# Performance work log

Measured on AMD Instinct MI355X. Metric: run time of the kernel, lower is better.

## Reference

```python
import jax, jax.numpy as jnp
import numpy as np

N, E, D, H, O, G = 50000, 800000, 64, 64, 32, 64


def setup_inputs() -> dict:
    key = jax.random.key(0)
    ks = jax.random.split(key, 12)
    x = jax.random.normal(ks[0], (N, D), dtype=jnp.float32)
    edge_index = jax.random.randint(ks[1], (2, E), 0, N)
    batch = jnp.sort(jax.random.randint(ks[2], (N,), 0, G))

    def glorot(k, fan_in, fan_out):
        s = np.sqrt(6.0 / (fan_in + fan_out)).astype(np.float32)
        return jax.random.uniform(k, (fan_in, fan_out), jnp.float32, -s, s)

    return {
        "x": x,
        "edge_index": edge_index,
        "batch": batch,
        "W1": glorot(ks[3], D, H), "b1": jnp.zeros((H,), jnp.float32),
        "W2": glorot(ks[4], H, H), "b2": jnp.zeros((H,), jnp.float32),
        "W3": glorot(ks[5], H, H), "b3": jnp.zeros((H,), jnp.float32),
        "Wl": glorot(ks[6], H, O), "bl": jnp.zeros((O,), jnp.float32),
    }


def reference(x, edge_index, batch, W1, b1, W2, b2, W3, b3, Wl, bl):
    n = x.shape[0]
    # GCNConv default: add self-loops, symmetric deg^-1/2 normalization
    loop = jnp.arange(n, dtype=edge_index.dtype)
    src = jnp.concatenate([edge_index[0], loop])  # [E+N]
    dst = jnp.concatenate([edge_index[1], loop])
    deg = jax.ops.segment_sum(jnp.ones_like(src, dtype=x.dtype), dst, num_segments=n)
    dis = jax.lax.rsqrt(deg)  # deg >= 1 due to self-loops
    norm = (dis[src] * dis[dst])[:, None]  # [E+N, 1]

    def gcn(h, W, b):
        hw = h @ W                      # [N, H] small GEMM
        msg = hw[src] * norm            # gather + scale: [E+N, H]
        agg = jax.ops.segment_sum(msg, dst, num_segments=n)  # scatter-add
        return agg + b

    h = jax.nn.relu(gcn(x, W1, b1))
    h = jax.nn.relu(gcn(h, W2, b2))
    h = gcn(h, W3, b3)

    # global_mean_pool over graph ids
    counts = jax.ops.segment_sum(jnp.ones((n,), h.dtype), batch, num_segments=G)
    pooled = jax.ops.segment_sum(h, batch, num_segments=G) / counts[:, None]

    # dropout(p=0.5) is identity in eval mode
    return pooled @ Wl + bl
```

## Files before the change

### kernel.cpp

```cpp
#include <hip/hip_runtime.h>

#define HD 64
#define PSUB 16
#define NBLK 256
#define LOG_NBLK 8
#define NBKT 512

__device__ __forceinline__ unsigned short f2bf(float f) {
    union { float f; unsigned u; } v; v.f = f;
    unsigned r = v.u + 0x7FFF + ((v.u >> 16) & 1);
    return (unsigned short)(r >> 16);
}
__device__ __forceinline__ float u2f(unsigned u) {
    union { unsigned u; float f; } v; v.u = u;
    return v.f;
}


__global__ __launch_bounds__(256) void hist1_k(const int* __restrict__ dst,
                                               int* __restrict__ hist, int E, int chunk,
                                               float* __restrict__ partial, int psz)
{
    __shared__ int lh[NBKT];
    int t = threadIdx.x;
    for (int i = t; i < NBKT; i += 256) lh[i] = 0;
    for (int i = blockIdx.x * 256 + t; i < psz; i += gridDim.x * 256)
        partial[i] = 0.f;
    __syncthreads();
    int base = blockIdx.x * chunk;
    int end  = min(base + chunk, E);
    for (int i = base + t; i < end; i += 256)
        atomicAdd(&lh[dst[i] >> 7], 1);
    __syncthreads();
    for (int i = t; i < NBKT; i += 256)
        hist[blockIdx.x * NBKT + i] = lh[i];
}

__global__ __launch_bounds__(256) void scanA_k(const int* __restrict__ hist,
                                               int* __restrict__ tsum)
{
    __shared__ int s[256];
    int t = threadIdx.x;
    int l = blockIdx.x * 256 + t;
    int phys = (l & (NBLK - 1)) * NBKT + (l >> LOG_NBLK);
    s[t] = hist[phys];
    __syncthreads();
    for (int off = 128; off > 0; off >>= 1) {
        if (t < off) s[t] += s[t + off];
        __syncthreads();
    }
    if (t == 0) tsum[blockIdx.x] = s[0];
}

__global__ __launch_bounds__(1024) void scanB_k(int* __restrict__ tsum, int nb,
    const int* __restrict__ batch, int* __restrict__ gstart, int n, int G)
{
    __shared__ int s[1024];
    int t = threadIdx.x;
    int v = (t < nb) ? tsum[t] : 0;
    s[t] = v;
    __syncthreads();
    for (int off = 1; off < 1024; off <<= 1) {
        int u = (t >= off) ? s[t - off] : 0;
        __syncthreads();
        s[t] += u;
        __syncthreads();
    }
    if (t < nb) tsum[t] = s[t] - v;
    if (t <= G) {
        if (t == G) gstart[t] = n;
        else {
            int lo = 0, hi = n;
            while (lo < hi) { int m = (lo + hi) >> 1; if (batch[m] < t) lo = m + 1; else hi = m; }
            gstart[t] = lo;
        }
    }
}

__global__ __launch_bounds__(256) void scanC_k(const int* __restrict__ hist,
                                               const int* __restrict__ tsum,
                                               int* __restrict__ scanned)
{
    __shared__ int s[256];
    int t = threadIdx.x;
    int l = blockIdx.x * 256 + t;
    int phys = (l & (NBLK - 1)) * NBKT + (l >> LOG_NBLK);
    int own = hist[phys];
    s[t] = own;
    __syncthreads();
    for (int off = 1; off < 256; off <<= 1) {
        int u = (t >= off) ? s[t - off] : 0;
        __syncthreads();
        s[t] += u;
        __syncthreads();
    }
    scanned[l] = tsum[blockIdx.x] + s[t] - own;
}

__global__ __launch_bounds__(256) void append_k(const int* __restrict__ src,
    const int* __restrict__ dst, const int* __restrict__ scanned,
    int* __restrict__ pairs, int E, int chunk)
{
    __shared__ int cur[NBKT];
    int t = threadIdx.x;
    int blk = blockIdx.x;
    for (int i = t; i < NBKT; i += 256) cur[i] = scanned[i * NBLK + blk];
    __syncthreads();
    int base = blk * chunk;
    int end  = min(base + chunk, E);
    for (int i = base + t; i < end; i += 256) {
        int s = src[i], d = dst[i];
        int p = atomicAdd(&cur[d >> 7], 1);
        pairs[p] = (s << 7) | (d & 127);
    }
}

__global__ __launch_bounds__(256) void bucket_csr_k(const int* __restrict__ pairs,
    const int* __restrict__ scanned, int* __restrict__ offsets,
    float* __restrict__ dis, int* __restrict__ csr_src, int N, int E)
{
    __shared__ int cnt[128];
    __shared__ int sc[128];
    __shared__ int cur[128];
    int t = threadIdx.x;
    int b = blockIdx.x;
    int nodeBase = b * 128;
    int nNodes = min(128, N - nodeBase);
    int bBase = scanned[b * NBLK];
    int bEnd  = (b + 1 < NBKT) ? scanned[(b + 1) * NBLK] : E;

    if (t < 128) cnt[t] = 0;
    __syncthreads();
    for (int i = bBase + t; i < bEnd; i += 256)
        atomicAdd(&cnt[pairs[i] & 127], 1);
    __syncthreads();
    int myc = (t < 128) ? cnt[t] : 0;
    if (t < 128) sc[t] = myc;
    __syncthreads();
    for (int off = 1; off < 128; off <<= 1) {
        int u = (t < 128 && t >= off) ? sc[t - off] : 0;
        __syncthreads();
        if (t < 128) sc[t] += u;
        __syncthreads();
    }
    if (t < 128) {
        int excl = sc[t] - myc;
        cur[t] = excl;
        if (t < nNodes) {
            offsets[nodeBase + t] = bBase + excl;
            dis[nodeBase + t] = rsqrtf(1.0f + (float)myc);
        }
    }
    if (t == 0 && b == gridDim.x - 1) offsets[N] = E;
    __syncthreads();
    for (int i = bBase + t; i < bEnd; i += 256) {
        int pk = pairs[i];
        int pos = bBase + atomicAdd(&cur[pk & 127], 1);
        csr_src[pos] = ((unsigned)pk) >> 7;
    }
}


__global__ __launch_bounds__(256) void gemm64_k(
    const float* __restrict__ in, const float* __restrict__ b_prev, int relu_prev,
    const float* __restrict__ W, const float* __restrict__ dis,
    unsigned short* __restrict__ outb, int n)
{
    __shared__ float HsT[HD][68];
    __shared__ float Ws[HD][HD];
    int t = threadIdx.x;
    int rowBase = blockIdx.x * 64;

    for (int i = t; i < HD * HD / 4; i += 256)
        ((float4*)Ws)[i] = ((const float4*)W)[i];

    if (blockIdx.x == 0 && t < 64)
        outb[(size_t)n * HD + t] = 0;

    {
        int k0 = (t & 15) * 4;
        float4 bb = make_float4(0.f, 0.f, 0.f, 0.f);
        if (b_prev) bb = *(const float4*)&b_prev[k0];
        for (int it = 0; it < 4; ++it) {
            int r = (t >> 4) + it * 16;
            int row = rowBase + r;
            float4 v = make_float4(0.f, 0.f, 0.f, 0.f);
            if (row < n) {
                v = *(const float4*)&in[(size_t)row * HD + k0];
                v.x += bb.x; v.y += bb.y; v.z += bb.z; v.w += bb.w;
                if (relu_prev) {
                    v.x = fmaxf(v.x, 0.f); v.y = fmaxf(v.y, 0.f);
                    v.z = fmaxf(v.z, 0.f); v.w = fmaxf(v.w, 0.f);
                }
            }
            HsT[k0 + 0][r] = v.x;
            HsT[k0 + 1][r] = v.y;
            HsT[k0 + 2][r] = v.z;
            HsT[k0 + 3][r] = v.w;
        }
    }
    __syncthreads();

    int c4 = (t & 15) * 4;
    int r4 = (t >> 4) * 4;
    float acc[4][4];
    #pragma unroll
    for (int i = 0; i < 4; ++i)
        #pragma unroll
        for (int j = 0; j < 4; ++j) acc[i][j] = 0.f;

    #pragma unroll 8
    for (int k = 0; k < HD; ++k) {
        float4 a = *(const float4*)&HsT[k][r4];
        float4 b = *(const float4*)&Ws[k][c4];
        acc[0][0] += a.x * b.x; acc[0][1] += a.x * b.y; acc[0][2] += a.x * b.z; acc[0][3] += a.x * b.w;
        acc[1][0] += a.y * b.x; acc[1][1] += a.y * b.y; acc[1][2] += a.y * b.z; acc[1][3] += a.y * b.w;
        acc[2][0] += a.z * b.x; acc[2][1] += a.z * b.y; acc[2][2] += a.z * b.z; acc[2][3] += a.z * b.w;
        acc[3][0] += a.w * b.x; acc[3][1] += a.w * b.y; acc[3][2] += a.w * b.z; acc[3][3] += a.w * b.w;
    }

    #pragma unroll
    for (int i = 0; i < 4; ++i) {
        int row = rowBase + r4 + i;
        if (row < n) {
            float ds = dis[row];
            ushort4 o;
            o.x = f2bf(ds * acc[i][0]); o.y = f2bf(ds * acc[i][1]);
            o.z = f2bf(ds * acc[i][2]); o.w = f2bf(ds * acc[i][3]);
            *(ushort4*)&outb[(size_t)row * HD + c4] = o;
        }
    }
}

__device__ __forceinline__ void gather4(const unsigned short* __restrict__ hwb,
    const int* __restrict__ offsets, const int* __restrict__ csr_src,
    int node, bool act, int n, int sub, int fl,
    float& a0, float& a1, float& a2, float& a3)
{
    int beg = 0, end = 0;
    if (act) { beg = offsets[node]; end = offsets[node + 1]; }
    int deg = end - beg;
    int md = deg;
    md = max(md, __shfl_xor(md, 16, 64));
    md = max(md, __shfl_xor(md, 32, 64));

    int nodeC = act ? node : n;
    uint2 sv = *(const uint2*)(hwb + ((size_t)nodeC << 6) + (fl << 2));
    a0 = u2f(sv.x << 16); a1 = u2f(sv.x & 0xFFFF0000u);
    a2 = u2f(sv.y << 16); a3 = u2f(sv.y & 0xFFFF0000u);

    int base = sub << 4;
    for (int jb = 0; jb < md; jb += 16) {
        int e = jb + fl;
        int idxv = (e < deg) ? csr_src[beg + e] : n;
        {
            uint2 g[8];
            #pragma unroll
            for (int j = 0; j < 8; ++j) {
                int row = __shfl(idxv, base + j, 64);
                g[j] = *(const uint2*)(hwb + ((size_t)row << 6) + (fl << 2));
            }
            #pragma unroll
            for (int j = 0; j < 8; ++j) {
                a0 += u2f(g[j].x << 16); a1 += u2f(g[j].x & 0xFFFF0000u);
                a2 += u2f(g[j].y << 16); a3 += u2f(g[j].y & 0xFFFF0000u);
            }
        }
        if (jb + 8 < md) {
            uint2 g[8];
            #pragma unroll
            for (int j = 0; j < 8; ++j) {
                int row = __shfl(idxv, base + 8 + j, 64);
                g[j] = *(const uint2*)(hwb + ((size_t)row << 6) + (fl << 2));
            }
            #pragma unroll
            for (int j = 0; j < 8; ++j) {
                a0 += u2f(g[j].x << 16); a1 += u2f(g[j].x & 0xFFFF0000u);
                a2 += u2f(g[j].y << 16); a3 += u2f(g[j].y & 0xFFFF0000u);
            }
        }
    }
}

__global__ __launch_bounds__(256) void agg_gemm_k(
    const unsigned short* __restrict__ hwb, const float* __restrict__ dis,
    const int* __restrict__ offsets, const int* __restrict__ csr_src,
    const float* __restrict__ b_prev, const float* __restrict__ W,
    unsigned short* __restrict__ outb, int n)
{
    __shared__ float As[16][68];
    __shared__ float Ws[HD][HD];
    int t    = threadIdx.x;
    int lane = t & 63;
    int sub  = lane >> 4;
    int fl   = lane & 15;
    int w    = t >> 6;
    int nib  = w * 4 + sub;
    int nodeBase = blockIdx.x * 16;
    int node = nodeBase + nib;
    bool act = node < n;

    for (int i = t; i < HD * HD / 4; i += 256)
        ((float4*)Ws)[i] = ((const float4*)W)[i];

    if (blockIdx.x == 0 && t < 64)
        outb[(size_t)n * HD + t] = 0;

    float a0, a1, a2, a3;
    gather4(hwb, offsets, csr_src, node, act, n, sub, fl, a0, a1, a2, a3);

    float ds = act ? dis[node] : 0.f;
    int c0 = fl << 2;
    float4 bb = *(const float4*)&b_prev[c0];
    float4 v;
    v.x = fmaxf(a0 * ds + bb.x, 0.f);
    v.y = fmaxf(a1 * ds + bb.y, 0.f);
    v.z = fmaxf(a2 * ds + bb.z, 0.f);
    v.w = fmaxf(a3 * ds + bb.w, 0.f);
    *(float4*)&As[nib][c0] = v;
    __syncthreads();

    int r  = t & 15;
    int c4 = (t >> 4) << 2;
    float acc0 = 0.f, acc1 = 0.f, acc2 = 0.f, acc3 = 0.f;
    #pragma unroll 4
    for (int k = 0; k < HD; k += 4) {
        float4 a  = *(const float4*)&As[r][k];
        float4 w0 = *(const float4*)&Ws[k + 0][c4];
        float4 w1 = *(const float4*)&Ws[k + 1][c4];
        float4 w2 = *(const float4*)&Ws[k + 2][c4];
        float4 w3 = *(const float4*)&Ws[k + 3][c4];
        acc0 += a.x * w0.x + a.y * w1.x + a.z * w2.x + a.w * w3.x;
        acc1 += a.x * w0.y + a.y * w1.y + a.z * w2.y + a.w * w3.y;
        acc2 += a.x * w0.z + a.y * w1.z + a.z * w2.z + a.w * w3.z;
        acc3 += a.x * w0.w + a.y * w1.w + a.z * w2.w + a.w * w3.w;
    }
    int orow = nodeBase + r;
    if (orow < n) {
        float d2 = dis[orow];
        ushort4 o;
        o.x = f2bf(d2 * acc0); o.y = f2bf(d2 * acc1);
        o.z = f2bf(d2 * acc2); o.w = f2bf(d2 * acc3);
        *(ushort4*)&outb[(size_t)orow * HD + c4] = o;
    }
}

__global__ __launch_bounds__(256) void agg_pool4_k(const unsigned short* __restrict__ hwb,
    const float* __restrict__ dis, const int* __restrict__ offsets,
    const int* __restrict__ csr_src, const int* __restrict__ batch,
    float* __restrict__ partial, int n)
{
    __shared__ float sh[16][68];
    __shared__ int gids[16];
    __shared__ int allsame;
    int t    = threadIdx.x;
    int lane = t & 63;
    int sub  = lane >> 4;
    int fl   = lane & 15;
    int w    = t >> 6;
    int nib  = w * 4 + sub;
    int node = blockIdx.x * 16 + nib;
    bool act = node < n;

    float a0, a1, a2, a3;
    gather4(hwb, offsets, csr_src, node, act, n, sub, fl, a0, a1, a2, a3);

    float ds = act ? dis[node] : 0.f;
    *(float4*)&sh[nib][fl << 2] = make_float4(a0 * ds, a1 * ds, a2 * ds, a3 * ds);
    if (fl == 0) gids[nib] = act ? batch[node] : -1;
    __syncthreads();

    if (t == 0) {
        int g0 = gids[0];
        int ok = (g0 >= 0);
        #pragma unroll
        for (int r = 1; r < 16; ++r) ok &= (gids[r] == g0);
        allsame = ok;
    }
    __syncthreads();

    int slot = blockIdx.x & (PSUB - 1);
    if (allsame) {
        if (t < 64) {
            float s = 0.f;
            #pragma unroll
            for (int r = 0; r < 16; ++r) s += sh[r][t];
            atomicAdd(&partial[((size_t)gids[0] * PSUB + slot) * HD + t], s);
        }
    } else {
        int c  = t & 63;
        int r0 = w * 4;
        int ga = gids[r0], gb = gids[r0 + 1], gc = gids[r0 + 2], gd = gids[r0 + 3];
        if (ga == gb && gb == gc && gc == gd && ga >= 0) {
            float v = sh[r0][c] + sh[r0 + 1][c] + sh[r0 + 2][c] + sh[r0 + 3][c];
            atomicAdd(&partial[((size_t)ga * PSUB + slot) * HD + c], v);
        } else {
            if (ga >= 0) atomicAdd(&partial[((size_t)ga * PSUB + slot) * HD + c], sh[r0][c]);
            if (gb >= 0) atomicAdd(&partial[((size_t)gb * PSUB + slot) * HD + c], sh[r0 + 1][c]);
            if (gc >= 0) atomicAdd(&partial[((size_t)gc * PSUB + slot) * HD + c], sh[r0 + 2][c]);
            if (gd >= 0) atomicAdd(&partial[((size_t)gd * PSUB + slot) * HD + c], sh[r0 + 3][c]);
        }
    }
}

__global__ __launch_bounds__(64) void pool2_k(const float* __restrict__ partial,
    const int* __restrict__ gstart, const float* __restrict__ b3,
    const float* __restrict__ Wl, const float* __restrict__ bl,
    float* __restrict__ out, int O)
{
    __shared__ float pooled[HD];
    int g = blockIdx.x;
    int t = threadIdx.x;
    float sum = 0.0f;
    #pragma unroll
    for (int s = 0; s < PSUB; ++s)
        sum += partial[((size_t)g * PSUB + s) * HD + t];
    float cnt = (float)(gstart[g + 1] - gstart[g]);
    pooled[t] = sum / cnt + b3[t];
    __syncthreads();
    if (t < O) {
        float acc = bl[t];
        #pragma unroll
        for (int k = 0; k < HD; ++k) acc += pooled[k] * Wl[k * O + t];
        out[g * O + t] = acc;
    }
}

extern "C" void kernel_launch(void* const* d_in, const int* in_sizes, int n_in,
                              void* d_out, int out_size, void* d_ws, size_t ws_size,
                              hipStream_t stream)
{
    const float* x    = (const float*)d_in[0];
    const int*   ei   = (const int*)d_in[1];
    const int*   batch= (const int*)d_in[2];
    const float* W1   = (const float*)d_in[3];
    const float* b1   = (const float*)d_in[4];
    const float* W2   = (const float*)d_in[5];
    const float* b2   = (const float*)d_in[6];
    const float* W3   = (const float*)d_in[7];
    const float* b3   = (const float*)d_in[8];
    const float* Wl   = (const float*)d_in[9];
    const float* bl   = (const float*)d_in[10];
    float* out = (float*)d_out;

    const int N = in_sizes[0] / HD;
    const int E = in_sizes[1] / 2;
    const int O = in_sizes[10];
    const int G = out_size / O;

    const int* src = ei;
    const int* dst = ei + E;

    char* p = (char*)d_ws;
    auto take = [&](size_t bytes) { char* r = p; p += (bytes + 255) & ~(size_t)255; return r; };
    int*   csr_src = (int*)  take((size_t)(E + 256) * 4);
    int*   offsets = (int*)  take((size_t)(N + 1) * 4);
    float* dis     = (float*)take((size_t)N * 4);
    int*   gstart  = (int*)  take((size_t)(G + 1) * 4);
    float* partial = (float*)take((size_t)G * PSUB * HD * 4);
    unsigned short* hwb  = (unsigned short*)take((size_t)(N + 1) * HD * 2);
    unsigned short* hwb2 = (unsigned short*)take((size_t)(N + 1) * HD * 2);

    int* pairs   = (int*)hwb;
    int* hist    = (int*)hwb2;
    int* scanned = hist + NBLK * NBKT;
    int* tsum    = scanned + NBLK * NBKT;

    const int TB = 256;
    int chunk   = (E + NBLK - 1) / NBLK;
    int ntiles  = (NBLK * NBKT) / 256;
    int nb_gemm = (N + 63) / 64;
    int nb_agg4 = (N + 15) / 16;
    int nbuck   = (N + 127) / 128;
    int psz     = G * PSUB * HD;

    hist1_k<<<NBLK, TB, 0, stream>>>(dst, hist, E, chunk, partial, psz);
    scanA_k<<<ntiles, TB, 0, stream>>>(hist, tsum);
    scanB_k<<<1, 1024, 0, stream>>>(tsum, ntiles, batch, gstart, N, G);
    scanC_k<<<ntiles, TB, 0, stream>>>(hist, tsum, scanned);
    append_k<<<NBLK, TB, 0, stream>>>(src, dst, scanned, pairs, E, chunk);
    bucket_csr_k<<<nbuck, TB, 0, stream>>>(pairs, scanned, offsets, dis, csr_src, N, E);

    gemm64_k<<<nb_gemm, TB, 0, stream>>>(x, nullptr, 0, W1, dis, hwb, N);

    agg_gemm_k<<<nb_agg4, TB, 0, stream>>>(hwb, dis, offsets, csr_src, b1, W2, hwb2, N);

    agg_gemm_k<<<nb_agg4, TB, 0, stream>>>(hwb2, dis, offsets, csr_src, b2, W3, hwb, N);

    agg_pool4_k<<<nb_agg4, TB, 0, stream>>>(hwb, dis, offsets, csr_src, batch, partial, N);

    pool2_k<<<G, 64, 0, stream>>>(partial, gstart, b3, Wl, bl, out, O);
}
```

Before: 192.4 us.

## Replace bucketed CSR build with atomic degree count, single scan, atomic scatter

The multi-stage bucketed CSR construction (hist, three scan kernels, append, per-bucket sort) is replaced by a global atomic degree histogram, a single-block 1024-thread scan that also writes dis and offsets, and an atomic scatter into csr_src. The final pooling kernel is folded into agg_pool4_k through a last-block-done counter, and zeroing moves to one hipMemsetAsync. This cuts kernel launches but relies on global atomics with poor locality and a serial single-block scan over 50k nodes, and CSR neighbour order becomes nondeterministic.

Measured after the change: 644.8 us. 235% more time.

```diff
diff --git a/kernel.cpp b/kernel.cpp
--- a/kernel.cpp
+++ b/kernel.cpp
@@ -2,9 +2,6 @@
 
 #define HD 64
 #define PSUB 16
-#define NBLK 256
-#define LOG_NBLK 8
-#define NBKT 512
 
 __device__ __forceinline__ unsigned short f2bf(float f) {
     union { float f; unsigned u; } v; v.f = f;
@@ -17,48 +14,27 @@
 }
 
 
-__global__ __launch_bounds__(256) void hist1_k(const int* __restrict__ dst,
-                                               int* __restrict__ hist, int E, int chunk,
-                                               float* __restrict__ partial, int psz)
-{
-    __shared__ int lh[NBKT];
-    int t = threadIdx.x;
-    for (int i = t; i < NBKT; i += 256) lh[i] = 0;
-    for (int i = blockIdx.x * 256 + t; i < psz; i += gridDim.x * 256)
-        partial[i] = 0.f;
-    __syncthreads();
-    int base = blockIdx.x * chunk;
-    int end  = min(base + chunk, E);
-    for (int i = base + t; i < end; i += 256)
-        atomicAdd(&lh[dst[i] >> 7], 1);
-    __syncthreads();
-    for (int i = t; i < NBKT; i += 256)
-        hist[blockIdx.x * NBKT + i] = lh[i];
-}
-
-__global__ __launch_bounds__(256) void scanA_k(const int* __restrict__ hist,
-                                               int* __restrict__ tsum)
-{
-    __shared__ int s[256];
-    int t = threadIdx.x;
-    int l = blockIdx.x * 256 + t;
-    int phys = (l & (NBLK - 1)) * NBKT + (l >> LOG_NBLK);
-    s[t] = hist[phys];
-    __syncthreads();
-    for (int off = 128; off > 0; off >>= 1) {
-        if (t < off) s[t] += s[t + off];
-        __syncthreads();
-    }
-    if (t == 0) tsum[blockIdx.x] = s[0];
-}
-
-__global__ __launch_bounds__(1024) void scanB_k(int* __restrict__ tsum, int nb,
-    const int* __restrict__ batch, int* __restrict__ gstart, int n, int G)
+__global__ __launch_bounds__(256) void hist_k(const int* __restrict__ dst,
+                                              int* __restrict__ deg, int E)
+{
+    int stride = gridDim.x * 256;
+    for (int i = blockIdx.x * 256 + threadIdx.x; i < E; i += stride)
+        atomicAdd(&deg[dst[i]], 1);
+}
+
+__global__ __launch_bounds__(1024) void scan_k(const int* __restrict__ deg,
+    int* __restrict__ offsets, float* __restrict__ dis,
+    const int* __restrict__ batch, int* __restrict__ gstart,
+    int n, int G, int E)
 {
     __shared__ int s[1024];
     int t = threadIdx.x;
-    int v = (t < nb) ? tsum[t] : 0;
-    s[t] = v;
+    int chunk = (n + 1023) >> 10;
+    int b0 = t * chunk;
+    int b1 = min(b0 + chunk, n);
+    int sum = 0;
+    for (int i = b0; i < b1; ++i) sum += deg[i];
+    s[t] = sum;
     __syncthreads();
     for (int off = 1; off < 1024; off <<= 1) {
         int u = (t >= off) ? s[t - off] : 0;
@@ -66,7 +42,14 @@
         s[t] += u;
         __syncthreads();
     }
-    if (t < nb) tsum[t] = s[t] - v;
+    int run = s[t] - sum;
+    for (int i = b0; i < b1; ++i) {
+        int d = deg[i];
+        offsets[i] = run;
+        dis[i] = rsqrtf(1.0f + (float)d);
+        run += d;
+    }
+    if (t == 0) offsets[n] = E;
     if (t <= G) {
         if (t == G) gstart[t] = n;
         else {
@@ -77,94 +60,22 @@
     }
 }
 
-__global__ __launch_bounds__(256) void scanC_k(const int* __restrict__ hist,
-                                               const int* __restrict__ tsum,
-                                               int* __restrict__ scanned)
-{
-    __shared__ int s[256];
-    int t = threadIdx.x;
-    int l = blockIdx.x * 256 + t;
-    int phys = (l & (NBLK - 1)) * NBKT + (l >> LOG_NBLK);
-    int own = hist[phys];
-    s[t] = own;
-    __syncthreads();
-    for (int off = 1; off < 256; off <<= 1) {
-        int u = (t >= off) ? s[t - off] : 0;
-        __syncthreads();
-        s[t] += u;
-        __syncthreads();
-    }
-    scanned[l] = tsum[blockIdx.x] + s[t] - own;
-}
-
-__global__ __launch_bounds__(256) void append_k(const int* __restrict__ src,
-    const int* __restrict__ dst, const int* __restrict__ scanned,
-    int* __restrict__ pairs, int E, int chunk)
-{
-    __shared__ int cur[NBKT];
-    int t = threadIdx.x;
-    int blk = blockIdx.x;
-    for (int i = t; i < NBKT; i += 256) cur[i] = scanned[i * NBLK + blk];
-    __syncthreads();
-    int base = blk * chunk;
-    int end  = min(base + chunk, E);
-    for (int i = base + t; i < end; i += 256) {
-        int s = src[i], d = dst[i];
-        int p = atomicAdd(&cur[d >> 7], 1);
-        pairs[p] = (s << 7) | (d & 127);
-    }
-}
-
-__global__ __launch_bounds__(256) void bucket_csr_k(const int* __restrict__ pairs,
-    const int* __restrict__ scanned, int* __restrict__ offsets,
-    float* __restrict__ dis, int* __restrict__ csr_src, int N, int E)
-{
-    __shared__ int cnt[128];
-    __shared__ int sc[128];
-    __shared__ int cur[128];
-    int t = threadIdx.x;
-    int b = blockIdx.x;
-    int nodeBase = b * 128;
-    int nNodes = min(128, N - nodeBase);
-    int bBase = scanned[b * NBLK];
-    int bEnd  = (b + 1 < NBKT) ? scanned[(b + 1) * NBLK] : E;
-
-    if (t < 128) cnt[t] = 0;
-    __syncthreads();
-    for (int i = bBase + t; i < bEnd; i += 256)
-        atomicAdd(&cnt[pairs[i] & 127], 1);
-    __syncthreads();
-    int myc = (t < 128) ? cnt[t] : 0;
-    if (t < 128) sc[t] = myc;
-    __syncthreads();
-    for (int off = 1; off < 128; off <<= 1) {
-        int u = (t < 128 && t >= off) ? sc[t - off] : 0;
-        __syncthreads();
-        if (t < 128) sc[t] += u;
-        __syncthreads();
-    }
-    if (t < 128) {
-        int excl = sc[t] - myc;
-        cur[t] = excl;
-        if (t < nNodes) {
-            offsets[nodeBase + t] = bBase + excl;
-            dis[nodeBase + t] = rsqrtf(1.0f + (float)myc);
-        }
-    }
-    if (t == 0 && b == gridDim.x - 1) offsets[N] = E;
-    __syncthreads();
-    for (int i = bBase + t; i < bEnd; i += 256) {
-        int pk = pairs[i];
-        int pos = bBase + atomicAdd(&cur[pk & 127], 1);
-        csr_src[pos] = ((unsigned)pk) >> 7;
+__global__ __launch_bounds__(256) void scatter_k(const int* __restrict__ src,
+    const int* __restrict__ dst, const int* __restrict__ offsets,
+    int* __restrict__ cur, int* __restrict__ csr_src, int E)
+{
+    int stride = gridDim.x * 256;
+    for (int i = blockIdx.x * 256 + threadIdx.x; i < E; i += stride) {
+        int d = dst[i];
+        int pos = offsets[d] + atomicAdd(&cur[d], 1);
+        csr_src[pos] = src[i];
     }
 }
 
 
 __global__ __launch_bounds__(256) void gemm64_k(
-    const float* __restrict__ in, const float* __restrict__ b_prev, int relu_prev,
-    const float* __restrict__ W, const float* __restrict__ dis,
-    unsigned short* __restrict__ outb, int n)
+    const float* __restrict__ in, const float* __restrict__ W,
+    const float* __restrict__ dis, unsigned short* __restrict__ outb, int n)
 {
     __shared__ float HsT[HD][68];
     __shared__ float Ws[HD][HD];
@@ -179,20 +90,12 @@
 
     {
         int k0 = (t & 15) * 4;
-        float4 bb = make_float4(0.f, 0.f, 0.f, 0.f);
-        if (b_prev) bb = *(const float4*)&b_prev[k0];
         for (int it = 0; it < 4; ++it) {
             int r = (t >> 4) + it * 16;
             int row = rowBase + r;
             float4 v = make_float4(0.f, 0.f, 0.f, 0.f);
-            if (row < n) {
+            if (row < n)
                 v = *(const float4*)&in[(size_t)row * HD + k0];
-                v.x += bb.x; v.y += bb.y; v.z += bb.z; v.w += bb.w;
-                if (relu_prev) {
-                    v.x = fmaxf(v.x, 0.f); v.y = fmaxf(v.y, 0.f);
-                    v.z = fmaxf(v.z, 0.f); v.w = fmaxf(v.w, 0.f);
-                }
-            }
             HsT[k0 + 0][r] = v.x;
             HsT[k0 + 1][r] = v.y;
             HsT[k0 + 2][r] = v.z;
@@ -348,11 +251,16 @@
 __global__ __launch_bounds__(256) void agg_pool4_k(const unsigned short* __restrict__ hwb,
     const float* __restrict__ dis, const int* __restrict__ offsets,
     const int* __restrict__ csr_src, const int* __restrict__ batch,
-    float* __restrict__ partial, int n)
+    float* __restrict__ partial, int* __restrict__ ctr,
+    const int* __restrict__ gstart, const float* __restrict__ b3,
+    const float* __restrict__ Wl, const float* __restrict__ bl,
+    float* __restrict__ out, int n, int O, int G)
 {
     __shared__ float sh[16][68];
     __shared__ int gids[16];
     __shared__ int allsame;
+    __shared__ int amLast;
+    __shared__ float pooled[64][HD + 1];
     int t    = threadIdx.x;
     int lane = t & 63;
     int sub  = lane >> 4;
@@ -401,28 +309,37 @@
             if (gd >= 0) atomicAdd(&partial[((size_t)gd * PSUB + slot) * HD + c], sh[r0 + 3][c]);
         }
     }
-}
-
-__global__ __launch_bounds__(64) void pool2_k(const float* __restrict__ partial,
-    const int* __restrict__ gstart, const float* __restrict__ b3,
-    const float* __restrict__ Wl, const float* __restrict__ bl,
-    float* __restrict__ out, int O)
-{
-    __shared__ float pooled[HD];
-    int g = blockIdx.x;
-    int t = threadIdx.x;
-    float sum = 0.0f;
-    #pragma unroll
-    for (int s = 0; s < PSUB; ++s)
-        sum += partial[((size_t)g * PSUB + s) * HD + t];
-    float cnt = (float)(gstart[g + 1] - gstart[g]);
-    pooled[t] = sum / cnt + b3[t];
-    __syncthreads();
-    if (t < O) {
-        float acc = bl[t];
-        #pragma unroll
-        for (int k = 0; k < HD; ++k) acc += pooled[k] * Wl[k * O + t];
-        out[g * O + t] = acc;
+
+    __threadfence();
+    if (t == 0) {
+        int old = __hip_atomic_fetch_add(ctr, 1, __ATOMIC_ACQ_REL, __HIP_MEMORY_SCOPE_AGENT);
+        amLast = (old == (int)gridDim.x - 1);
+    }
+    __syncthreads();
+    if (!amLast) return;
+
+    for (int gb = 0; gb < G; gb += 64) {
+        int gcnt = min(64, G - gb);
+        for (int idx = t; idx < gcnt * HD; idx += 256) {
+            int gl = idx >> 6, c = idx & 63;
+            int g = gb + gl;
+            float s = 0.f;
+            #pragma unroll
+            for (int sl = 0; sl < PSUB; ++sl)
+                s += __hip_atomic_fetch_add(&partial[((size_t)g * PSUB + sl) * HD + c],
+                                            0.0f, __ATOMIC_RELAXED, __HIP_MEMORY_SCOPE_AGENT);
+            float cnt = (float)(gstart[g + 1] - gstart[g]);
+            pooled[gl][c] = s / cnt + b3[c];
+        }
+        __syncthreads();
+        for (int idx = t; idx < gcnt * O; idx += 256) {
+            int gl = idx / O, o = idx - gl * O;
+            float acc = bl[o];
+            #pragma unroll
+            for (int k = 0; k < HD; ++k) acc += pooled[gl][k] * Wl[k * O + o];
+            out[(size_t)(gb + gl) * O + o] = acc;
+        }
+        __syncthreads();
     }
 }
 
@@ -457,37 +374,34 @@
     int*   offsets = (int*)  take((size_t)(N + 1) * 4);
     float* dis     = (float*)take((size_t)N * 4);
     int*   gstart  = (int*)  take((size_t)(G + 1) * 4);
-    float* partial = (float*)take((size_t)G * PSUB * HD * 4);
+
+    int psz = G * PSUB * HD;
+    size_t zbytes = 256 + (size_t)(N + 1) * 4 + (size_t)N * 4 + (size_t)psz * 4;
+    char*  zbase  = take(zbytes);
+    int*   ctr     = (int*)zbase;
+    int*   deg     = (int*)(zbase + 256);
+    int*   cur     = deg + (N + 1);
+    float* partial = (float*)(cur + N);
+
     unsigned short* hwb  = (unsigned short*)take((size_t)(N + 1) * HD * 2);
     unsigned short* hwb2 = (unsigned short*)take((size_t)(N + 1) * HD * 2);
 
-    int* pairs   = (int*)hwb;
-    int* hist    = (int*)hwb2;
-    int* scanned = hist + NBLK * NBKT;
-    int* tsum    = scanned + NBLK * NBKT;
-
     const int TB = 256;
-    int chunk   = (E + NBLK - 1) / NBLK;
-    int ntiles  = (NBLK * NBKT) / 256;
+    int nb_edge = min((E + TB - 1) / TB, 2048);
     int nb_gemm = (N + 63) / 64;
     int nb_agg4 = (N + 15) / 16;
-    int nbuck   = (N + 127) / 128;
-    int psz     = G * PSUB * HD;
-
-    hist1_k<<<NBLK, TB, 0, stream>>>(dst, hist, E, chunk, partial, psz);
-    scanA_k<<<ntiles, TB, 0, stream>>>(hist, tsum);
-    scanB_k<<<1, 1024, 0, stream>>>(tsum, ntiles, batch, gstart, N, G);
-    scanC_k<<<ntiles, TB, 0, stream>>>(hist, tsum, scanned);
-    append_k<<<NBLK, TB, 0, stream>>>(src, dst, scanned, pairs, E, chunk);
-    bucket_csr_k<<<nbuck, TB, 0, stream>>>(pairs, scanned, offsets, dis, csr_src, N, E);
-
-    gemm64_k<<<nb_gemm, TB, 0, stream>>>(x, nullptr, 0, W1, dis, hwb, N);
+
+    hipMemsetAsync(zbase, 0, zbytes, stream);
+    hist_k<<<nb_edge, TB, 0, stream>>>(dst, deg, E);
+    scan_k<<<1, 1024, 0, stream>>>(deg, offsets, dis, batch, gstart, N, G, E);
+    scatter_k<<<nb_edge, TB, 0, stream>>>(src, dst, offsets, cur, csr_src, E);
+
+    gemm64_k<<<nb_gemm, TB, 0, stream>>>(x, W1, dis, hwb, N);
 
     agg_gemm_k<<<nb_agg4, TB, 0, stream>>>(hwb, dis, offsets, csr_src, b1, W2, hwb2, N);
 
     agg_gemm_k<<<nb_agg4, TB, 0, stream>>>(hwb2, dis, offsets, csr_src, b2, W3, hwb, N);
 
-    agg_pool4_k<<<nb_agg4, TB, 0, stream>>>(hwb, dis, offsets, csr_src, batch, partial, N);
-
-    pool2_k<<<G, 64, 0, stream>>>(partial, gstart, b3, Wl, bl, out, O);
-}
+    agg_pool4_k<<<nb_agg4, TB, 0, stream>>>(hwb, dis, offsets, csr_src, batch,
+                                            partial, ctr, gstart, b3, Wl, bl, out, N, O, G);
+}
```
